# Performance work log

Hardware: AMD Instinct MI355X
Metric: run time of the kernel (lower is better)

## Reference

```python
import jax, jax.numpy as jnp
import numpy as np

N_NODES = 40000
N_EDGES = 640000
D = 64          # node feature dim / out_features
HEADS = 4
K2 = 64         # n_grid_K**3
BN_EPS = 1e-5
SEG_EPS = 1e-16
R_EPS = 1e-8


def segment_softmax(alpha, seg, num_segments):
    # alpha: [E, H], seg: [E] int
    seg_max = jax.ops.segment_max(alpha, seg, num_segments=num_segments)
    seg_max = jnp.where(jnp.isfinite(seg_max), seg_max, 0.0)
    a = jnp.exp(alpha - seg_max[seg])
    denom = jax.ops.segment_sum(a, seg, num_segments=num_segments)
    return a / (denom[seg] + SEG_EPS)


def setup_inputs() -> dict:
    key = jax.random.key(0)
    ks = jax.random.split(key, 12)
    inp = {}
    inp["input"] = jax.random.normal(ks[0], (N_NODES, D), dtype=jnp.float32)
    inp["rij"] = jax.random.uniform(ks[1], (N_EDGES,), dtype=jnp.float32)
    inp["plane_wave"] = jax.random.normal(ks[2], (N_EDGES, K2), dtype=jnp.float32)
    inp["edge_attr"] = jax.random.normal(ks[3], (N_EDGES, D), dtype=jnp.float32)
    # learned parameters (torch Linear(in,out,bias=False) -> [in,out] here)
    def glorot(k, shape):
        fan = shape[0] + shape[-1]
        s = jnp.sqrt(6.0 / fan)
        return jax.random.uniform(k, shape, minval=-s, maxval=s, dtype=jnp.float32)
    inp["Wg"] = glorot(ks[4], (3 * D, D))          # linear_gate 192->64
    inp["Wm"] = glorot(ks[5], (3 * D, D))          # linear_MLP 192->64
    inp["W2"] = glorot(ks[6], (K2, D))             # linear2_vector
    inp["W2g"] = glorot(ks[7], (K2, K2))           # linear2_vector_gate
    inp["Wa"] = glorot(ks[8], (2 * D, HEADS * D))  # AGAT W
    inp["att"] = glorot(ks[9], (1, HEADS, 2 * D))  # AGAT att
    inp["bn_gamma"] = jnp.ones((HEADS,), dtype=jnp.float32)
    inp["bn_beta"] = jnp.zeros((HEADS,), dtype=jnp.float32)
    # graph indices
    src = jax.random.randint(ks[10], (N_EDGES,), 0, N_NODES, dtype=jnp.int32)
    tgt = jax.random.randint(ks[11], (N_EDGES,), 0, N_NODES, dtype=jnp.int32)
    inp["edge_sources"] = src
    inp["edge_targets"] = tgt
    inp["edge_index"] = jnp.stack([src, tgt], axis=0)
    inp["nodes"] = jnp.zeros((1,), dtype=jnp.int32)  # unused in forward
    return inp


def reference(input, rij, plane_wave, edge_attr, Wg, Wm, W2, W2g, Wa, att,
              bn_gamma, bn_beta, nodes, edge_sources, edge_targets, edge_index):
    # gated edge MLP branch
    ni = input[edge_sources]                       # [E, D]
    nj = input[edge_targets]                       # [E, D]
    r = rij + (rij == 0).astype(rij.dtype) * R_EPS
    delta = (ni - nj) / r[:, None]
    final_fe = jnp.concatenate([ni, nj, delta], axis=1)   # [E, 3D]
    e_gate = jax.nn.sigmoid(final_fe @ Wg)                 # [E, D]
    e_mlp = jax.nn.elu(final_fe @ Wm)                      # [E, D]
    # plane-wave gated linear branch
    gate = jax.nn.sigmoid(plane_wave @ W2g)                # [E, K2]
    z2 = (plane_wave * gate) @ W2                          # [E, D]
    # AGAT branch (eval-mode BatchNorm1d: running mean 0, var 1)
    row, col = edge_index[0], edge_index[1]
    out_i = jax.nn.softplus(jnp.concatenate([input[row], edge_attr], axis=1) @ Wa)
    out_j = jax.nn.softplus(jnp.concatenate([input[col], edge_attr], axis=1) @ Wa)
    out_i = out_i.reshape(-1, HEADS, D)                    # [E, H, D]
    out_j = out_j.reshape(-1, HEADS, D)
    alpha = jax.nn.softplus((jnp.concatenate([out_i, out_j], axis=-1) * att).sum(-1))  # [E, H]
    alpha = jax.nn.softplus(alpha / jnp.sqrt(1.0 + BN_EPS) * bn_gamma + bn_beta)
    alpha = segment_softmax(alpha, row, N_NODES)
    z1 = (out_j * alpha[:, :, None]).mean(axis=1)          # mean over heads -> [E, D]
    # combine + scatter-add
    z = e_gate * e_mlp * (z1 + z2)
    output = input.at[edge_sources].add(z)
    return output
```

## Files before the change

### kernel.cpp

```cpp
#include <hip/hip_runtime.h>
#include <math.h>

#define N_NODES 40000
#define N_EDGES 640000
#define NT0 16

typedef short short8 __attribute__((ext_vector_type(8)));
typedef unsigned short ushort8v __attribute__((ext_vector_type(8)));
typedef unsigned short ushort4v __attribute__((ext_vector_type(4)));
typedef float fragC __attribute__((ext_vector_type(4)));

__device__ __forceinline__ float softplus_f(float x) {
    return x > 15.f ? x : __logf(1.f + __expf(x));
}
__device__ __forceinline__ float sigmoid_f(float x) {
    return 1.f / (1.f + __expf(-x));
}
__device__ __forceinline__ short f2bf(float f) {
    unsigned u = __float_as_uint(f);
    u += 0x7FFF + ((u >> 16) & 1);
    return (short)(u >> 16);
}
__device__ __forceinline__ float bf2f(unsigned short u) {
    return __uint_as_float(((unsigned)u) << 16);
}

__global__ void k_weights(const float* __restrict__ Wa, const float* __restrict__ W2g,
                          const float* __restrict__ W2, short* __restrict__ WaTb,
                          short* __restrict__ W2gTb, short* __restrict__ W2Tb) {
    int idx = blockIdx.x * blockDim.x + threadIdx.x;
    int stride = gridDim.x * blockDim.x;
    for (int i = idx; i < 256 * 64; i += stride) {
        int c = i >> 6, k = i & 63;
        WaTb[i] = f2bf(Wa[(64 + k) * 256 + c]);
    }
    for (int i = idx; i < 64 * 64; i += stride) {
        int c = i >> 6, k = i & 63;
        W2gTb[i] = f2bf(W2g[k * 64 + c]);
        W2Tb[i]  = f2bf(W2[k * 64 + c]);
    }
}

__global__ __launch_bounds__(256) void k_node_pre(const float* __restrict__ X,
                                                  const float* __restrict__ Wg,
                                                  const float* __restrict__ Wm,
                                                  const float* __restrict__ Wa,
                                                  short* __restrict__ nodeAxaT,
                                                  short* __restrict__ nodeGT,
                                                  float* __restrict__ nodeDT) {
    __shared__ float xs[NT0 * 64];
    int t = threadIdx.x;
    int n0 = blockIdx.x * NT0;
    ((float4*)xs)[t] = ((const float4*)(X + (size_t)n0 * 64))[t];
    __syncthreads();
    for (int c = t; c < 640; c += 256) {
        const float* wptr;
        int ld;
        if (c < 192)      { wptr = Wg + (c >> 6) * 64 * 64 + (c & 63); ld = 64; }
        else if (c < 384) { wptr = Wm + ((c - 192) >> 6) * 64 * 64 + (c & 63); ld = 64; }
        else              { wptr = Wa + (c - 384); ld = 256; }
        float acc[NT0];
#pragma unroll
        for (int n = 0; n < NT0; n++) acc[n] = 0.f;
        for (int kc = 0; kc < 16; kc++) {
            float w0 = wptr[(4 * kc + 0) * ld];
            float w1 = wptr[(4 * kc + 1) * ld];
            float w2 = wptr[(4 * kc + 2) * ld];
            float w3 = wptr[(4 * kc + 3) * ld];
#pragma unroll
            for (int n = 0; n < NT0; n++) {
                float4 x = ((float4*)xs)[n * 16 + kc];
                acc[n] += x.x * w0 + x.y * w1 + x.z * w2 + x.w * w3;
            }
        }
#pragma unroll
        for (int n = 0; n < NT0; n++) {
            float v = acc[n];
            size_t nn = (size_t)(n0 + n);
            if (c < 64) {
                nodeGT[nn * 256 + (c & 15) * 4 + (c >> 4)] = f2bf(v);
            } else if (c < 128) {
                int d = c - 64;  nodeGT[nn * 256 + 64 + (d & 15) * 4 + (d >> 4)] = f2bf(v);
            } else if (c < 192) {
                int d = c - 128; nodeDT[nn * 128 + (d & 15) * 4 + (d >> 4)] = v;
            } else if (c < 256) {
                int d = c - 192; nodeGT[nn * 256 + 128 + (d & 15) * 4 + (d >> 4)] = f2bf(v);
            } else if (c < 320) {
                int d = c - 256; nodeGT[nn * 256 + 192 + (d & 15) * 4 + (d >> 4)] = f2bf(v);
            } else if (c < 384) {
                int d = c - 320; nodeDT[nn * 128 + 64 + (d & 15) * 4 + (d >> 4)] = v;
            } else {
                int co = c - 384; nodeAxaT[nn * 256 + (co & 15) * 16 + (co >> 4)] = f2bf(v);
            }
        }
    }
}

__global__ __launch_bounds__(256) void k_alpha(
    const float* __restrict__ ea, const int* __restrict__ src, const int* __restrict__ tgt,
    const unsigned short* __restrict__ nodeAxaT, const short* __restrict__ WaTb,
    const float* __restrict__ att, const float* __restrict__ gamma,
    const float* __restrict__ beta,
    float* __restrict__ alphaBuf, float* __restrict__ segSum) {
    __shared__ short ldsW[256 * 72];
    __shared__ float attS[512];
    int t = threadIdx.x;
    {
        const float4* s4 = (const float4*)(WaTb + t * 64);
        float4* d4 = (float4*)(ldsW + t * 72);
#pragma unroll
        for (int k = 0; k < 8; k++) d4[k] = s4[k];
        attS[t] = att[(t >> 6) * 128 + (t & 63)];
        attS[256 + t] = att[(t >> 6) * 128 + 64 + (t & 63)];
    }
    __syncthreads();
    int wave = t >> 6, lane = t & 63;
    int i = lane & 15, q = lane >> 4;
    int eb = blockIdx.x * 64 + wave * 16;

    short8 afr[2];
    {
        const float* ap = ea + (size_t)(eb + i) * 64 + q * 8;
#pragma unroll
        for (int kt = 0; kt < 2; kt++) {
            float4 x0 = *(const float4*)(ap + kt * 32);
            float4 x1 = *(const float4*)(ap + kt * 32 + 4);
            short8 a;
            a[0] = f2bf(x0.x); a[1] = f2bf(x0.y); a[2] = f2bf(x0.z); a[3] = f2bf(x0.w);
            a[4] = f2bf(x1.x); a[5] = f2bf(x1.y); a[6] = f2bf(x1.z); a[7] = f2bf(x1.w);
            afr[kt] = a;
        }
    }
    int sI[4];
    ushort8v gs[4][2], gt[4][2];
#pragma unroll
    for (int r = 0; r < 4; r++) {
        int e = eb + q * 4 + r;
        sI[r] = src[e];
        int tg = tgt[e];
        const unsigned short* ps = nodeAxaT + (size_t)sI[r] * 256 + i * 16;
        const unsigned short* pt = nodeAxaT + (size_t)tg * 256 + i * 16;
        gs[r][0] = *(const ushort8v*)(ps);
        gs[r][1] = *(const ushort8v*)(ps + 8);
        gt[r][0] = *(const ushort8v*)(pt);
        gt[r][1] = *(const ushort8v*)(pt + 8);
    }
    float part[4][4];
#pragma unroll
    for (int h = 0; h < 4; h++)
#pragma unroll
        for (int r = 0; r < 4; r++) part[h][r] = 0.f;

#pragma unroll
    for (int nt = 0; nt < 16; nt++) {
        const short* wrow = ldsW + (nt * 16 + i) * 72 + q * 8;
        short8 b0 = *(const short8*)(wrow);
        short8 b1 = *(const short8*)(wrow + 32);
        fragC acc = {0.f, 0.f, 0.f, 0.f};
        acc = __builtin_amdgcn_mfma_f32_16x16x32_bf16(afr[0], b0, acc, 0, 0, 0);
        acc = __builtin_amdgcn_mfma_f32_16x16x32_bf16(afr[1], b1, acc, 0, 0, 0);
        float atti = attS[nt * 16 + i];
        float attj = attS[256 + nt * 16 + i];
        int h = nt >> 2;
#pragma unroll
        for (int r = 0; r < 4; r++) {
            float P = acc[r];
            float oi = softplus_f(bf2f(gs[r][nt >> 3][nt & 7]) + P);
            float oj = softplus_f(bf2f(gt[r][nt >> 3][nt & 7]) + P);
            part[h][r] += oi * atti + oj * attj;
        }
    }
    const float inv_s = 0.99999500003749968f;
#pragma unroll
    for (int r = 0; r < 4; r++) {
        float pr[4];
#pragma unroll
        for (int h = 0; h < 4; h++) {
            float p = part[h][r];
            p += __shfl_xor(p, 1);
            p += __shfl_xor(p, 2);
            p += __shfl_xor(p, 4);
            p += __shfl_xor(p, 8);
            pr[h] = p;
        }
        if (i == 0) {
            float av[4];
#pragma unroll
            for (int h = 0; h < 4; h++) {
                float araw = softplus_f(pr[h]);
                av[h] = __expf(softplus_f(araw * inv_s * gamma[h] + beta[h]));
            }
            int e = eb + q * 4 + r;
            *(float4*)(alphaBuf + (size_t)e * 4) = make_float4(av[0], av[1], av[2], av[3]);
            atomicAdd(&segSum[sI[r] * 4 + 0], av[0]);
            atomicAdd(&segSum[sI[r] * 4 + 1], av[1]);
            atomicAdd(&segSum[sI[r] * 4 + 2], av[2]);
            atomicAdd(&segSum[sI[r] * 4 + 3], av[3]);
        }
    }
}

__global__ __launch_bounds__(256) void k_final(
    const float* __restrict__ ea, const float* __restrict__ pw,
    const float* __restrict__ rij,
    const int* __restrict__ src, const int* __restrict__ tgt,
    const unsigned short* __restrict__ nodeAxaT, const unsigned short* __restrict__ nodeGT,
    const float* __restrict__ nodeDT,
    const short* __restrict__ WaTb, const short* __restrict__ W2gTb,
    const short* __restrict__ W2Tb,
    const float* __restrict__ alphaBuf, const float* __restrict__ segSum,
    float* __restrict__ out) {
    __shared__ short ldsW[256 * 72];
    int t = threadIdx.x;
    {
        const float4* s4 = (const float4*)(WaTb + t * 64);
        float4* d4 = (float4*)(ldsW + t * 72);
#pragma unroll
        for (int k = 0; k < 8; k++) d4[k] = s4[k];
    }
    int wave = t >> 6, lane = t & 63;
    int i = lane & 15, q = lane >> 4;
    int eb = blockIdx.x * 64 + wave * 16;

    int sI[4], tgI[4];
    float ir[4];
    float wal[4][4];
#pragma unroll
    for (int r = 0; r < 4; r++) {
        int e = eb + q * 4 + r;
        sI[r] = src[e];
        tgI[r] = tgt[e];
        float rr = rij[e];
        if (rr == 0.f) rr = 1e-8f;
        ir[r] = 1.f / rr;
        float4 av = *(const float4*)(alphaBuf + (size_t)e * 4);
        float4 sv = *(const float4*)(segSum + (size_t)sI[r] * 4);
        wal[r][0] = av.x / (sv.x + 1e-16f) * 0.25f;
        wal[r][1] = av.y / (sv.y + 1e-16f) * 0.25f;
        wal[r][2] = av.z / (sv.z + 1e-16f) * 0.25f;
        wal[r][3] = av.w / (sv.w + 1e-16f) * 0.25f;
    }

    short pg[4][4];
    {
        short8 pfr[2];
        const float* pp = pw + (size_t)(eb + i) * 64 + q * 8;
#pragma unroll
        for (int kt = 0; kt < 2; kt++) {
            float4 x0 = *(const float4*)(pp + kt * 32);
            float4 x1 = *(const float4*)(pp + kt * 32 + 4);
            short8 a;
            a[0] = f2bf(x0.x); a[1] = f2bf(x0.y); a[2] = f2bf(x0.z); a[3] = f2bf(x0.w);
            a[4] = f2bf(x1.x); a[5] = f2bf(x1.y); a[6] = f2bf(x1.z); a[7] = f2bf(x1.w);
            pfr[kt] = a;
        }
#pragma unroll
        for (int nt = 0; nt < 4; nt++) {
            const short* wrow = W2gTb + (nt * 16 + i) * 64 + q * 8;
            short8 b0 = *(const short8*)(wrow);
            short8 b1 = *(const short8*)(wrow + 32);
            fragC g = {0.f, 0.f, 0.f, 0.f};
            g = __builtin_amdgcn_mfma_f32_16x16x32_bf16(pfr[0], b0, g, 0, 0, 0);
            g = __builtin_amdgcn_mfma_f32_16x16x32_bf16(pfr[1], b1, g, 0, 0, 0);
            int k = nt * 16 + i;
#pragma unroll
            for (int r = 0; r < 4; r++) {
                float pv = pw[(size_t)(eb + q * 4 + r) * 64 + k];
                pg[nt][r] = f2bf(pv * sigmoid_f(g[r]));
            }
        }
    }

    ushort8v ga[4][2];
#pragma unroll
    for (int r = 0; r < 4; r++) {
        const unsigned short* pt = nodeAxaT + (size_t)tgI[r] * 256 + i * 16;
        ga[r][0] = *(const ushort8v*)(pt);
        ga[r][1] = *(const ushort8v*)(pt + 8);
    }

    __syncthreads();

    short8 afr[2];
    {
        const float* ap = ea + (size_t)(eb + i) * 64 + q * 8;
#pragma unroll
        for (int kt = 0; kt < 2; kt++) {
            float4 x0 = *(const float4*)(ap + kt * 32);
            float4 x1 = *(const float4*)(ap + kt * 32 + 4);
            short8 a;
            a[0] = f2bf(x0.x); a[1] = f2bf(x0.y); a[2] = f2bf(x0.z); a[3] = f2bf(x0.w);
            a[4] = f2bf(x1.x); a[5] = f2bf(x1.y); a[6] = f2bf(x1.z); a[7] = f2bf(x1.w);
            afr[kt] = a;
        }
    }
    float z1[4][4];
#pragma unroll
    for (int j = 0; j < 4; j++)
#pragma unroll
        for (int r = 0; r < 4; r++) z1[j][r] = 0.f;
#pragma unroll
    for (int nt = 0; nt < 16; nt++) {
        const short* wrow = ldsW + (nt * 16 + i) * 72 + q * 8;
        short8 b0 = *(const short8*)(wrow);
        short8 b1 = *(const short8*)(wrow + 32);
        fragC acc = {0.f, 0.f, 0.f, 0.f};
        acc = __builtin_amdgcn_mfma_f32_16x16x32_bf16(afr[0], b0, acc, 0, 0, 0);
        acc = __builtin_amdgcn_mfma_f32_16x16x32_bf16(afr[1], b1, acc, 0, 0, 0);
        int h = nt >> 2, j = nt & 3;
#pragma unroll
        for (int r = 0; r < 4; r++) {
            float oj = softplus_f(bf2f(ga[r][nt >> 3][nt & 7]) + acc[r]);
            z1[j][r] += oj * wal[r][h];
        }
    }

    __syncthreads();

    {
        short* pwgW = ldsW + wave * (16 * 72);
#pragma unroll
        for (int nt = 0; nt < 4; nt++)
#pragma unroll
            for (int r = 0; r < 4; r++)
                pwgW[(q * 4 + r) * 72 + nt * 16 + i] = pg[nt][r];
    }
    __syncthreads();

    short8 a2[2];
    {
        const short* prow = ldsW + wave * (16 * 72) + i * 72 + q * 8;
        a2[0] = *(const short8*)(prow);
        a2[1] = *(const short8*)(prow + 32);
    }
    fragC zt[4];
#pragma unroll
    for (int nt = 0; nt < 4; nt++) {
        const short* wrow = W2Tb + (nt * 16 + i) * 64 + q * 8;
        short8 b0 = *(const short8*)(wrow);
        short8 b1 = *(const short8*)(wrow + 32);
        fragC z = {z1[nt][0], z1[nt][1], z1[nt][2], z1[nt][3]};
        z = __builtin_amdgcn_mfma_f32_16x16x32_bf16(a2[0], b0, z, 0, 0, 0);
        z = __builtin_amdgcn_mfma_f32_16x16x32_bf16(a2[1], b1, z, 0, 0, 0);
        zt[nt] = z;
    }

#pragma unroll
    for (int r = 0; r < 4; r++) {
        const unsigned short* Gs = nodeGT + (size_t)sI[r] * 256;
        const unsigned short* Gt = nodeGT + (size_t)tgI[r] * 256;
        const float* Ds = nodeDT + (size_t)sI[r] * 128;
        const float* Dt = nodeDT + (size_t)tgI[r] * 128;
        ushort4v ag1 = *(const ushort4v*)(Gs + i * 4);
        ushort4v am1 = *(const ushort4v*)(Gs + 128 + i * 4);
        ushort4v ag2 = *(const ushort4v*)(Gt + 64 + i * 4);
        ushort4v am2 = *(const ushort4v*)(Gt + 192 + i * 4);
        float4 ag3s = *(const float4*)(Ds + i * 4);
        float4 am3s = *(const float4*)(Ds + 64 + i * 4);
        float4 ag3t = *(const float4*)(Dt + i * 4);
        float4 am3t = *(const float4*)(Dt + 64 + i * 4);
        float g3s[4] = {ag3s.x, ag3s.y, ag3s.z, ag3s.w};
        float m3s[4] = {am3s.x, am3s.y, am3s.z, am3s.w};
        float g3t[4] = {ag3t.x, ag3t.y, ag3t.z, ag3t.w};
        float m3t[4] = {am3t.x, am3t.y, am3t.z, am3t.w};
#pragma unroll
        for (int j = 0; j < 4; j++) {
            int d = j * 16 + i;
            float gl = bf2f(ag1[j]) + bf2f(ag2[j]) + (g3s[j] - g3t[j]) * ir[r];
            float ml = bf2f(am1[j]) + bf2f(am2[j]) + (m3s[j] - m3t[j]) * ir[r];
            float eg = sigmoid_f(gl);
            float em = ml > 0.f ? ml : (__expf(ml) - 1.f);
            float z = eg * em * (zt[j][r]);
            atomicAdd(&out[(size_t)sI[r] * 64 + d], z);
        }
    }
}

extern "C" void kernel_launch(void* const* d_in, const int* in_sizes, int n_in,
                              void* d_out, int out_size, void* d_ws, size_t ws_size,
                              hipStream_t stream) {
    const float* input = (const float*)d_in[0];
    const float* rij   = (const float*)d_in[1];
    const float* pw    = (const float*)d_in[2];
    const float* ea    = (const float*)d_in[3];
    const float* Wg    = (const float*)d_in[4];
    const float* Wm    = (const float*)d_in[5];
    const float* W2    = (const float*)d_in[6];
    const float* W2g   = (const float*)d_in[7];
    const float* Wa    = (const float*)d_in[8];
    const float* att   = (const float*)d_in[9];
    const float* gamma = (const float*)d_in[10];
    const float* beta  = (const float*)d_in[11];
    const int* srcIdx  = (const int*)d_in[12];
    const int* tgtIdx  = (const int*)d_in[13];
    float* out = (float*)d_out;

    char* wsb = (char*)d_ws;
    short* nodeAxaT = (short*)(wsb);
    short* nodeGT   = (short*)(wsb + 20480000);
    float* nodeDT   = (float*)(wsb + 40960000);
    float* alphaBuf = (float*)(wsb + 61440000);
    float* segSum   = (float*)(wsb + 71680000);
    short* WaTb     = (short*)(wsb + 72320000);
    short* W2gTb    = (short*)(wsb + 72352768);
    short* W2Tb     = (short*)(wsb + 72360960);

    hipMemsetAsync(wsb + 71680000, 0, 640000, stream);
    hipMemcpyAsync(d_out, (const void*)input, (size_t)N_NODES * 64 * sizeof(float),
                   hipMemcpyDeviceToDevice, stream);

    k_weights<<<32, 256, 0, stream>>>(Wa, W2g, W2, WaTb, W2gTb, W2Tb);
    k_node_pre<<<N_NODES / NT0, 256, 0, stream>>>(input, Wg, Wm, Wa,
                                                  nodeAxaT, nodeGT, nodeDT);
    k_alpha<<<N_EDGES / 64, 256, 0, stream>>>(ea, srcIdx, tgtIdx,
                                              (const unsigned short*)nodeAxaT, WaTb,
                                              att, gamma, beta, alphaBuf, segSum);
    k_final<<<N_EDGES / 64, 256, 0, stream>>>(ea, pw, rij, srcIdx, tgtIdx,
                                              (const unsigned short*)nodeAxaT,
                                              (const unsigned short*)nodeGT, nodeDT,
                                              WaTb, W2gTb, W2Tb, alphaBuf, segSum, out);
}
```

Baseline: 967.5 us.

## Reorder k_final stages with XOR-swizzled LDS and lower register pressure

Shrinks the shared-memory tile from padded 72-wide rows to 64-wide rows and uses an XOR swizzle to avoid bank conflicts. The gated plane-wave product is now written to LDS and read back before the Wa weights are loaded, so the pg register array no longer stays live. The target-node gathers are split into two halves, rij loading is moved next to its use, and launch bounds request 5 blocks per SM. The goal is lower VGPR and LDS use for higher occupancy, at the cost of an extra barrier and possible register spilling under the tighter bound.

```diff
diff --git a/kernel.cpp b/kernel.cpp
--- a/kernel.cpp
+++ b/kernel.cpp
@@ -200,7 +200,7 @@
     }
 }
 
-__global__ __launch_bounds__(256) void k_final(
+__global__ __launch_bounds__(256, 5) void k_final(
     const float* __restrict__ ea, const float* __restrict__ pw,
     const float* __restrict__ rij,
     const int* __restrict__ src, const int* __restrict__ tgt,
@@ -210,29 +210,20 @@
     const short* __restrict__ W2Tb,
     const float* __restrict__ alphaBuf, const float* __restrict__ segSum,
     float* __restrict__ out) {
-    __shared__ short ldsW[256 * 72];
+    __shared__ short ldsW[256 * 64];
     int t = threadIdx.x;
-    {
-        const float4* s4 = (const float4*)(WaTb + t * 64);
-        float4* d4 = (float4*)(ldsW + t * 72);
-#pragma unroll
-        for (int k = 0; k < 8; k++) d4[k] = s4[k];
-    }
     int wave = t >> 6, lane = t & 63;
     int i = lane & 15, q = lane >> 4;
+    int swz = i & 7;
     int eb = blockIdx.x * 64 + wave * 16;
 
     int sI[4], tgI[4];
-    float ir[4];
     float wal[4][4];
 #pragma unroll
     for (int r = 0; r < 4; r++) {
         int e = eb + q * 4 + r;
         sI[r] = src[e];
         tgI[r] = tgt[e];
-        float rr = rij[e];
-        if (rr == 0.f) rr = 1e-8f;
-        ir[r] = 1.f / rr;
         float4 av = *(const float4*)(alphaBuf + (size_t)e * 4);
         float4 sv = *(const float4*)(segSum + (size_t)sI[r] * 4);
         wal[r][0] = av.x / (sv.x + 1e-16f) * 0.25f;
@@ -241,7 +232,7 @@
         wal[r][3] = av.w / (sv.w + 1e-16f) * 0.25f;
     }
 
-    short pg[4][4];
+    short* wreg = ldsW + wave * 16 * 64;
     {
         short8 pfr[2];
         const float* pp = pw + (size_t)(eb + i) * 64 + q * 8;
@@ -263,22 +254,30 @@
             g = __builtin_amdgcn_mfma_f32_16x16x32_bf16(pfr[0], b0, g, 0, 0, 0);
             g = __builtin_amdgcn_mfma_f32_16x16x32_bf16(pfr[1], b1, g, 0, 0, 0);
             int k = nt * 16 + i;
+            int ck = k >> 3, wk = k & 7;
 #pragma unroll
             for (int r = 0; r < 4; r++) {
                 float pv = pw[(size_t)(eb + q * 4 + r) * 64 + k];
-                pg[nt][r] = f2bf(pv * sigmoid_f(g[r]));
+                int rr = q * 4 + r;
+                wreg[rr * 64 + ((ck ^ (rr & 7)) << 3) + wk] = f2bf(pv * sigmoid_f(g[r]));
             }
         }
     }
 
-    ushort8v ga[4][2];
-#pragma unroll
-    for (int r = 0; r < 4; r++) {
-        const unsigned short* pt = nodeAxaT + (size_t)tgI[r] * 256 + i * 16;
-        ga[r][0] = *(const ushort8v*)(pt);
-        ga[r][1] = *(const ushort8v*)(pt + 8);
-    }
-
+    short8 a2[2];
+    {
+        const short* arow = wreg + i * 64;
+        a2[0] = *(const short8*)(arow + ((q ^ swz) << 3));
+        a2[1] = *(const short8*)(arow + (((q + 4) ^ swz) << 3));
+    }
+    __syncthreads();
+
+    {
+        const float4* s4 = (const float4*)(WaTb + t * 64);
+#pragma unroll
+        for (int c = 0; c < 8; c++)
+            *(float4*)(ldsW + t * 64 + (((c ^ (t & 7)) << 3))) = s4[c];
+    }
     __syncthreads();
 
     short8 afr[2];
@@ -300,39 +299,29 @@
 #pragma unroll
         for (int r = 0; r < 4; r++) z1[j][r] = 0.f;
 #pragma unroll
-    for (int nt = 0; nt < 16; nt++) {
-        const short* wrow = ldsW + (nt * 16 + i) * 72 + q * 8;
-        short8 b0 = *(const short8*)(wrow);
-        short8 b1 = *(const short8*)(wrow + 32);
-        fragC acc = {0.f, 0.f, 0.f, 0.f};
-        acc = __builtin_amdgcn_mfma_f32_16x16x32_bf16(afr[0], b0, acc, 0, 0, 0);
-        acc = __builtin_amdgcn_mfma_f32_16x16x32_bf16(afr[1], b1, acc, 0, 0, 0);
-        int h = nt >> 2, j = nt & 3;
-#pragma unroll
-        for (int r = 0; r < 4; r++) {
-            float oj = softplus_f(bf2f(ga[r][nt >> 3][nt & 7]) + acc[r]);
-            z1[j][r] += oj * wal[r][h];
-        }
-    }
-
-    __syncthreads();
-
-    {
-        short* pwgW = ldsW + wave * (16 * 72);
-#pragma unroll
-        for (int nt = 0; nt < 4; nt++)
-#pragma unroll
-            for (int r = 0; r < 4; r++)
-                pwgW[(q * 4 + r) * 72 + nt * 16 + i] = pg[nt][r];
-    }
-    __syncthreads();
-
-    short8 a2[2];
-    {
-        const short* prow = ldsW + wave * (16 * 72) + i * 72 + q * 8;
-        a2[0] = *(const short8*)(prow);
-        a2[1] = *(const short8*)(prow + 32);
-    }
+    for (int half = 0; half < 2; half++) {
+        ushort8v ga[4];
+#pragma unroll
+        for (int r = 0; r < 4; r++)
+            ga[r] = *(const ushort8v*)(nodeAxaT + (size_t)tgI[r] * 256 + i * 16 + half * 8);
+#pragma unroll
+        for (int nn = 0; nn < 8; nn++) {
+            int nt = half * 8 + nn;
+            const short* wr = ldsW + (nt * 16 + i) * 64;
+            short8 b0 = *(const short8*)(wr + ((q ^ swz) << 3));
+            short8 b1 = *(const short8*)(wr + (((q + 4) ^ swz) << 3));
+            fragC acc = {0.f, 0.f, 0.f, 0.f};
+            acc = __builtin_amdgcn_mfma_f32_16x16x32_bf16(afr[0], b0, acc, 0, 0, 0);
+            acc = __builtin_amdgcn_mfma_f32_16x16x32_bf16(afr[1], b1, acc, 0, 0, 0);
+            int h = nt >> 2, j = nt & 3;
+#pragma unroll
+            for (int r = 0; r < 4; r++) {
+                float oj = softplus_f(bf2f(ga[r][nn]) + acc[r]);
+                z1[j][r] += oj * wal[r][h];
+            }
+        }
+    }
+
     fragC zt[4];
 #pragma unroll
     for (int nt = 0; nt < 4; nt++) {
@@ -347,6 +336,9 @@
 
 #pragma unroll
     for (int r = 0; r < 4; r++) {
+        float rr = rij[eb + q * 4 + r];
+        if (rr == 0.f) rr = 1e-8f;
+        float ir = 1.f / rr;
         const unsigned short* Gs = nodeGT + (size_t)sI[r] * 256;
         const unsigned short* Gt = nodeGT + (size_t)tgI[r] * 256;
         const float* Ds = nodeDT + (size_t)sI[r] * 128;
@@ -366,8 +358,8 @@
 #pragma unroll
         for (int j = 0; j < 4; j++) {
             int d = j * 16 + i;
-            float gl = bf2f(ag1[j]) + bf2f(ag2[j]) + (g3s[j] - g3t[j]) * ir[r];
-            float ml = bf2f(am1[j]) + bf2f(am2[j]) + (m3s[j] - m3t[j]) * ir[r];
+            float gl = bf2f(ag1[j]) + bf2f(ag2[j]) + (g3s[j] - g3t[j]) * ir;
+            float ml = bf2f(am1[j]) + bf2f(am2[j]) + (m3s[j] - m3t[j]) * ir;
             float eg = sigmoid_f(gl);
             float em = ml > 0.f ? ml : (__expf(ml) - 1.f);
             float z = eg * em * (zt[j][r]);
```

Result: slower. 1.233 ms (+27.4%).
